# Performance work log

Hardware: AMD Instinct MI355X
Metric: run time of the kernel (lower is better)

The kernel has to match this reference:

```python
import jax, jax.numpy as jnp
import numpy as np

N, C, H, W = 8, 32, 256, 256
DEPTH = 4
PAD = (1, 1, 2, 2, 1, 1)  # (w_l, w_r, h_t, h_b, d_f, d_b)
K = 2  # pool kernel/stride along each of D,H,W
EPS = 1e-5


def setup_inputs() -> dict:
    key = jax.random.key(0)
    k1, k2, k3, k4, k5 = jax.random.split(key, 5)
    x = jax.random.normal(k1, (N, C, H, W), dtype=jnp.float32)
    gamma = jax.random.normal(k2, (C,), dtype=jnp.float32) * 0.1 + 1.0
    beta = jax.random.normal(k3, (C,), dtype=jnp.float32) * 0.1
    conv_w = jax.random.normal(k4, (C, C), dtype=jnp.float32) / np.sqrt(C)  # 1x1 conv [out,in]
    conv_b = jax.random.normal(k5, (C,), dtype=jnp.float32) * 0.1
    return {"x": x, "gamma": gamma, "beta": beta, "conv_w": conv_w, "conv_b": conv_b}


def _forward(x, gamma, beta, conv_w, conv_b):
    n, c, h, w = x.shape
    # InstanceNorm2d (affine, biased variance, eps=1e-5), stats per (N,C) over H,W
    mean = jnp.mean(x, axis=(2, 3), keepdims=True)
    var = jnp.mean(jnp.square(x - mean), axis=(2, 3), keepdims=True)
    xn = (x - mean) * jax.lax.rsqrt(var + EPS)
    xn = xn * gamma[None, :, None, None] + beta[None, :, None, None]
    # expand to 5D by repeating along depth
    x3 = jnp.broadcast_to(xn[:, :, None, :, :], (n, c, DEPTH, h, w))
    # ConstantPad3d with value 0.0
    wl, wr, ht, hb, df, db = PAD
    xp = jnp.pad(x3, ((0, 0), (0, 0), (df, db), (ht, hb), (wl, wr)))
    Dp, Hp, Wp = DEPTH + df + db, h + ht + hb, w + wl + wr  # all even by construction
    dq, hq, wq = Dp // K, Hp // K, Wp // K
    # block view: [n,c,dq,K,hq,K,wq,K] -> [n,c,dq,hq,wq,K*K*K] (row-major window order,
    # matching PyTorch's flattened pooling-window index order)
    blk = xp.reshape(n, c, dq, K, hq, K, wq, K).transpose(0, 1, 2, 4, 6, 3, 5, 7)
    blk = blk.reshape(n, c, dq, hq, wq, K * K * K)
    mx = jnp.max(blk, axis=-1)
    idx = jnp.argmax(blk, axis=-1)  # first occurrence on ties, like PyTorch CPU
    # MaxUnpool3d: scatter max back to its argmax position, zeros elsewhere
    unp_blk = jax.nn.one_hot(idx, K * K * K, dtype=x.dtype) * mx[..., None]
    unpooled = unp_blk.reshape(n, c, dq, hq, wq, K, K, K).transpose(0, 1, 2, 5, 3, 6, 4, 7)
    unpooled = unpooled.reshape(n, c, Dp, Hp, Wp)
    # crop padding, collapse depth via mean
    cropped = unpooled[:, :, df:df + DEPTH, ht:ht + h, wl:wl + w]
    collapsed = jnp.mean(cropped, axis=2)  # [n,c,h,w]
    # 1x1 conv + relu
    out = jnp.einsum('oc,nchw->nohw', conv_w, collapsed) + conv_b[None, :, None, None]
    return jax.nn.relu(out)


def reference(x, gamma, beta, conv_w, conv_b):
    return _forward(x, gamma, beta, conv_w, conv_b)
```

## Files before the change

kernel.cpp:

```cpp
#include <hip/hip_runtime.h>

#define N_   8
#define C_   32
#define H_   256
#define W_   256
#define HW_  (H_ * W_)

__global__ __launch_bounds__(1024) void stats_kernel(
    const float* __restrict__ x, const float* __restrict__ gamma,
    const float* __restrict__ beta, float2* __restrict__ ss)
{
    const int nc = blockIdx.x;
    const int t  = threadIdx.x;
    const float4* p = (const float4*)(x + (size_t)nc * HW_);

    float s0 = 0.f, s1 = 0.f, s2 = 0.f, s3 = 0.f;
    float q0 = 0.f, q1 = 0.f, q2 = 0.f, q3 = 0.f;
    #pragma unroll
    for (int i = 0; i < 16; ++i) {
        float4 v = p[t + (i << 10)];
        s0 += v.x; s1 += v.y; s2 += v.z; s3 += v.w;
        q0 = fmaf(v.x, v.x, q0); q1 = fmaf(v.y, v.y, q1);
        q2 = fmaf(v.z, v.z, q2); q3 = fmaf(v.w, v.w, q3);
    }
    double s = (double)s0 + (double)s1 + (double)s2 + (double)s3;
    double q = (double)q0 + (double)q1 + (double)q2 + (double)q3;
    #pragma unroll
    for (int off = 32; off > 0; off >>= 1) {
        s += __shfl_down(s, off);
        q += __shfl_down(q, off);
    }
    __shared__ double rs[16], rq[16];
    const int wid = t >> 6;
    if ((t & 63) == 0) { rs[wid] = s; rq[wid] = q; }
    __syncthreads();
    if (t == 0) {
        double S = 0.0, Q = 0.0;
        #pragma unroll
        for (int i = 0; i < 16; ++i) { S += rs[i]; Q += rq[i]; }
        double mean = S / (double)HW_;
        double var  = Q / (double)HW_ - mean * mean;
        double grs  = (double)gamma[nc & (C_ - 1)] / sqrt(var + 1e-5);
        float scale = (float)grs;
        float shift = (float)((double)beta[nc & (C_ - 1)] - mean * grs);
        ss[nc] = make_float2(scale, shift);
    }
}

__global__ __launch_bounds__(256, 8) void fused_kernel(
    const float* __restrict__ x, const float2* __restrict__ ss,
    const float* __restrict__ Wm, const float* __restrict__ bias,
    float* __restrict__ out)
{
    const int k   = blockIdx.x;
    const int qtr = blockIdx.y;
    const int n   = blockIdx.z;
    const int t   = threadIdx.x;
    const int w0  = qtr << 6;

    __shared__ float         sWT[C_][36];
    __shared__ float         sV[C_][34];
    __shared__ unsigned char sP[C_][36];

    #pragma unroll
    for (int r = 0; r < 4; ++r) {
        int i = t + (r << 8);
        sWT[i & 31][i >> 5] = Wm[i];
    }

    const int c  = t >> 3;
    const int li = t & 7;
    const float2 sc = ss[n * C_ + c];
    const float* plane = x + (size_t)(n * C_ + c) * HW_ + (size_t)(2 * k) * W_;
    const float* rowb  = plane + w0 + 8 * li;
    float4 u00 = ((const float4*)rowb)[0];
    float4 u01 = ((const float4*)rowb)[1];
    float4 u10 = ((const float4*)(rowb + W_))[0];
    float4 u11 = ((const float4*)(rowb + W_))[1];

    float bm = 0.f; int br = 0;
    {
        bool needL = (li == 0) && (qtr > 0);
        bool needR = (li == 7) && (qtr < 3);
        if (needL || needR) {
            const float* bp = plane + (needL ? (w0 - 1) : (w0 + 64));
            float p0 = fmaf(bp[0],  sc.x, sc.y);
            float p1 = fmaf(bp[W_], sc.x, sc.y);
            bm = fmaxf(p0, p1); br = (p1 > p0) ? 1 : 0;
        }
    }

    float vm[8];
    unsigned vr = 0;
    {
        float a0, a1;
        a0 = fmaf(u00.x, sc.x, sc.y); a1 = fmaf(u10.x, sc.x, sc.y);
        vm[0] = fmaxf(a0, a1); if (a1 > a0) vr |= 1u << 0;
        a0 = fmaf(u00.y, sc.x, sc.y); a1 = fmaf(u10.y, sc.x, sc.y);
        vm[1] = fmaxf(a0, a1); if (a1 > a0) vr |= 1u << 1;
        a0 = fmaf(u00.z, sc.x, sc.y); a1 = fmaf(u10.z, sc.x, sc.y);
        vm[2] = fmaxf(a0, a1); if (a1 > a0) vr |= 1u << 2;
        a0 = fmaf(u00.w, sc.x, sc.y); a1 = fmaf(u10.w, sc.x, sc.y);
        vm[3] = fmaxf(a0, a1); if (a1 > a0) vr |= 1u << 3;
        a0 = fmaf(u01.x, sc.x, sc.y); a1 = fmaf(u11.x, sc.x, sc.y);
        vm[4] = fmaxf(a0, a1); if (a1 > a0) vr |= 1u << 4;
        a0 = fmaf(u01.y, sc.x, sc.y); a1 = fmaf(u11.y, sc.x, sc.y);
        vm[5] = fmaxf(a0, a1); if (a1 > a0) vr |= 1u << 5;
        a0 = fmaf(u01.z, sc.x, sc.y); a1 = fmaf(u11.z, sc.x, sc.y);
        vm[6] = fmaxf(a0, a1); if (a1 > a0) vr |= 1u << 6;
        a0 = fmaf(u01.w, sc.x, sc.y); a1 = fmaf(u11.w, sc.x, sc.y);
        vm[7] = fmaxf(a0, a1); if (a1 > a0) vr |= 1u << 7;
    }

    const float pvm = __shfl_up(vm[7], 1);
    const int   pvr = __shfl_up((int)((vr >> 7) & 1u), 1);

    #pragma unroll
    for (int b = 0; b < 4; ++b) {
        float vL; int rL; bool padL = false;
        if (b == 0) {
            if (li == 0) {
                if (qtr == 0) { vL = 0.f; rL = 0; padL = true; }
                else          { vL = bm;  rL = br; }
            } else { vL = pvm; rL = pvr; }
        } else {
            vL = vm[2 * b - 1]; rL = (int)((vr >> (2 * b - 1)) & 1u);
        }
        float vR = vm[2 * b]; int rR = (int)((vr >> (2 * b)) & 1u);
        bool chooseL = (vL > vR) || ((vL == vR) && (rL <= rR));
        float m   = chooseL ? vL : vR;
        int   p   = chooseL ? (rL << 1) : ((rR << 1) | 1);
        float val = m * (m > 0.f ? 0.75f : 0.25f);
        if (chooseL && padL) val = 0.f;
        int jl = 4 * li + b;
        sV[c][jl] = val;
        sP[c][jl] = (unsigned char)p;
    }
    if (li == 7) {
        float vL = vm[7]; int rL = (int)((vr >> 7) & 1u);
        float vR; int rR; bool padR;
        if (qtr < 3) { vR = bm;  rR = br; padR = false; }
        else         { vR = 0.f; rR = 0;  padR = true;  }
        bool chooseL = (vL > vR) || ((vL == vR) && (rL <= rR));
        float m   = chooseL ? vL : vR;
        int   p   = chooseL ? (rL << 1) : ((rR << 1) | 1);
        float val = m * (m > 0.f ? 0.75f : 0.25f);
        if (!chooseL && padR) val = 0.f;
        sV[c][32] = val;
        sP[c][32] = (unsigned char)p;
    }
    __syncthreads();

    const int wv = t >> 6;
    const int ob = wv << 3;
    const int L  = t & 63;
    const int jl = (L + 1) >> 1;
    const int pm0 = (L & 1) ? 0 : 1;

    float acc0[8], acc1[8];
    #pragma unroll
    for (int oo = 0; oo < 8; ++oo) {
        float bo = bias[ob + oo];
        acc0[oo] = bo; acc1[oo] = bo;
    }

    #pragma unroll 8
    for (int cc = 0; cc < C_; ++cc) {
        float v = sV[cc][jl];
        int   p = sP[cc][jl];
        float m0 = (p == pm0)     ? v : 0.f;
        float m1 = (p == pm0 + 2) ? v : 0.f;
        float4 wa = *(const float4*)&sWT[cc][ob];
        float4 wb = *(const float4*)&sWT[cc][ob + 4];
        acc0[0] = fmaf(m0, wa.x, acc0[0]);
        acc0[1] = fmaf(m0, wa.y, acc0[1]);
        acc0[2] = fmaf(m0, wa.z, acc0[2]);
        acc0[3] = fmaf(m0, wa.w, acc0[3]);
        acc0[4] = fmaf(m0, wb.x, acc0[4]);
        acc0[5] = fmaf(m0, wb.y, acc0[5]);
        acc0[6] = fmaf(m0, wb.z, acc0[6]);
        acc0[7] = fmaf(m0, wb.w, acc0[7]);
        acc1[0] = fmaf(m1, wa.x, acc1[0]);
        acc1[1] = fmaf(m1, wa.y, acc1[1]);
        acc1[2] = fmaf(m1, wa.z, acc1[2]);
        acc1[3] = fmaf(m1, wa.w, acc1[3]);
        acc1[4] = fmaf(m1, wb.x, acc1[4]);
        acc1[5] = fmaf(m1, wb.y, acc1[5]);
        acc1[6] = fmaf(m1, wb.z, acc1[6]);
        acc1[7] = fmaf(m1, wb.w, acc1[7]);
    }

    float* obase = out + (size_t)(n * C_ + ob) * HW_
                       + (size_t)(2 * k) * W_ + w0 + L;
    #pragma unroll
    for (int oo = 0; oo < 8; ++oo) {
        obase[(size_t)oo * HW_]      = fmaxf(acc0[oo], 0.f);
        obase[(size_t)oo * HW_ + W_] = fmaxf(acc1[oo], 0.f);
    }
}

extern "C" void kernel_launch(void* const* d_in, const int* in_sizes, int n_in,
                              void* d_out, int out_size, void* d_ws, size_t ws_size,
                              hipStream_t stream) {
    const float* x     = (const float*)d_in[0];
    const float* gamma = (const float*)d_in[1];
    const float* beta  = (const float*)d_in[2];
    const float* Wm    = (const float*)d_in[3];
    const float* bias  = (const float*)d_in[4];
    float* out  = (float*)d_out;
    float2* ss  = (float2*)d_ws;

    stats_kernel<<<N_ * C_, 1024, 0, stream>>>(x, gamma, beta, ss);
    fused_kernel<<<dim3(H_ / 2, 4, N_), 256, 0, stream>>>(x, ss, Wm, bias, out);
}
```

Baseline: 138.0 us.

## Precompute raw-value pooling maxima in stats pass to halve second-pass input reads

The stats kernel now also does the vertical and horizontal 2-way max/argmax on the raw (un-normalized) input and writes a quarter-size intermediate, with the 2-bit window position packed into the low mantissa bits. The second kernel reads this compact buffer instead of the full input and applies the per-channel scale/shift afterward. This relies on the affine normalization preserving order, which requires a positive scale (gamma > 0). The intent is to cut pass-2 global reads of x by about 4x, at the cost of an extra workspace write and read and a small loss of mantissa precision.

```diff
diff --git a/kernel.cpp b/kernel.cpp
--- a/kernel.cpp
+++ b/kernel.cpp
@@ -5,26 +5,82 @@
 #define H_   256
 #define W_   256
 #define HW_  (H_ * W_)
+#define BROW_ 132
+#define B_OFF_ 1024
 
-__global__ __launch_bounds__(1024) void stats_kernel(
+__device__ __forceinline__ float pack_vp(float m, int pos) {
+    return __uint_as_float((__float_as_uint(m) & ~3u) | (unsigned)pos);
+}
+
+__global__ __launch_bounds__(1024) void pass1_kernel(
     const float* __restrict__ x, const float* __restrict__ gamma,
-    const float* __restrict__ beta, float2* __restrict__ ss)
+    const float* __restrict__ beta, float* __restrict__ ws)
 {
     const int nc = blockIdx.x;
     const int t  = threadIdx.x;
-    const float4* p = (const float4*)(x + (size_t)nc * HW_);
+    const int li = t & 31;
+    const int k0 = t >> 5;
+    const float* plane = x + (size_t)nc * HW_;
+    float* Bp = ws + B_OFF_ + (size_t)nc * (128 * BROW_);
 
-    float s0 = 0.f, s1 = 0.f, s2 = 0.f, s3 = 0.f;
-    float q0 = 0.f, q1 = 0.f, q2 = 0.f, q3 = 0.f;
+    float sx=0.f, sy=0.f, sz=0.f, sw=0.f;
+    float qx=0.f, qy=0.f, qz=0.f, qw=0.f;
+
     #pragma unroll
-    for (int i = 0; i < 16; ++i) {
-        float4 v = p[t + (i << 10)];
-        s0 += v.x; s1 += v.y; s2 += v.z; s3 += v.w;
-        q0 = fmaf(v.x, v.x, q0); q1 = fmaf(v.y, v.y, q1);
-        q2 = fmaf(v.z, v.z, q2); q3 = fmaf(v.w, v.w, q3);
+    for (int p = 0; p < 4; ++p) {
+        const int k = k0 + 32 * p;
+        const float* r0 = plane + (size_t)(2 * k) * W_ + 8 * li;
+        float4 a0 = ((const float4*)r0)[0];
+        float4 a1 = ((const float4*)r0)[1];
+        float4 b0 = ((const float4*)(r0 + W_))[0];
+        float4 b1 = ((const float4*)(r0 + W_))[1];
+
+        sx += a0.x + a1.x + b0.x + b1.x;
+        sy += a0.y + a1.y + b0.y + b1.y;
+        sz += a0.z + a1.z + b0.z + b1.z;
+        sw += a0.w + a1.w + b0.w + b1.w;
+        qx = fmaf(a0.x,a0.x,qx); qx = fmaf(a1.x,a1.x,qx);
+        qx = fmaf(b0.x,b0.x,qx); qx = fmaf(b1.x,b1.x,qx);
+        qy = fmaf(a0.y,a0.y,qy); qy = fmaf(a1.y,a1.y,qy);
+        qy = fmaf(b0.y,b0.y,qy); qy = fmaf(b1.y,b1.y,qy);
+        qz = fmaf(a0.z,a0.z,qz); qz = fmaf(a1.z,a1.z,qz);
+        qz = fmaf(b0.z,b0.z,qz); qz = fmaf(b1.z,b1.z,qz);
+        qw = fmaf(a0.w,a0.w,qw); qw = fmaf(a1.w,a1.w,qw);
+        qw = fmaf(b0.w,b0.w,qw); qw = fmaf(b1.w,b1.w,qw);
+
+        float vm0 = fmaxf(a0.x, b0.x); int r0b = (b0.x > a0.x) ? 1 : 0;
+        float vm1 = fmaxf(a0.y, b0.y); int r1b = (b0.y > a0.y) ? 1 : 0;
+        float vm2 = fmaxf(a0.z, b0.z); int r2b = (b0.z > a0.z) ? 1 : 0;
+        float vm3 = fmaxf(a0.w, b0.w); int r3b = (b0.w > a0.w) ? 1 : 0;
+        float vm4 = fmaxf(a1.x, b1.x); int r4b = (b1.x > a1.x) ? 1 : 0;
+        float vm5 = fmaxf(a1.y, b1.y); int r5b = (b1.y > a1.y) ? 1 : 0;
+        float vm6 = fmaxf(a1.z, b1.z); int r6b = (b1.z > a1.z) ? 1 : 0;
+        float vm7 = fmaxf(a1.w, b1.w); int r7b = (b1.w > a1.w) ? 1 : 0;
+
+        const float pvm = __shfl_up(vm7, 1);
+        const int   pvr = __shfl_up(r7b, 1);
+
+        float f0, f1, f2, f3;
+        if (li == 0) {
+            f0 = pack_vp(vm0, (r0b << 1) | 1);
+        } else {
+            bool cl = (pvm > vm0) || ((pvm == vm0) && (pvr <= r0b));
+            f0 = cl ? pack_vp(pvm, pvr << 1) : pack_vp(vm0, (r0b << 1) | 1);
+        }
+        { bool cl = (vm1 > vm2) || ((vm1 == vm2) && (r1b <= r2b));
+          f1 = cl ? pack_vp(vm1, r1b << 1) : pack_vp(vm2, (r2b << 1) | 1); }
+        { bool cl = (vm3 > vm4) || ((vm3 == vm4) && (r3b <= r4b));
+          f2 = cl ? pack_vp(vm3, r3b << 1) : pack_vp(vm4, (r4b << 1) | 1); }
+        { bool cl = (vm5 > vm6) || ((vm5 == vm6) && (r5b <= r6b));
+          f3 = cl ? pack_vp(vm5, r5b << 1) : pack_vp(vm6, (r6b << 1) | 1); }
+
+        *(float4*)(Bp + (size_t)k * BROW_ + 4 * li) = make_float4(f0, f1, f2, f3);
+        if (li == 31)
+            Bp[(size_t)k * BROW_ + 128] = pack_vp(vm7, r7b << 1);
     }
-    double s = (double)s0 + (double)s1 + (double)s2 + (double)s3;
-    double q = (double)q0 + (double)q1 + (double)q2 + (double)q3;
+
+    double s = (double)sx + (double)sy + (double)sz + (double)sw;
+    double q = (double)qx + (double)qy + (double)qz + (double)qw;
     #pragma unroll
     for (int off = 32; off > 0; off >>= 1) {
         s += __shfl_down(s, off);
@@ -41,121 +97,46 @@
         double mean = S / (double)HW_;
         double var  = Q / (double)HW_ - mean * mean;
         double grs  = (double)gamma[nc & (C_ - 1)] / sqrt(var + 1e-5);
-        float scale = (float)grs;
-        float shift = (float)((double)beta[nc & (C_ - 1)] - mean * grs);
-        ss[nc] = make_float2(scale, shift);
+        ((float2*)ws)[nc] = make_float2((float)grs,
+                                        (float)((double)beta[nc & (C_ - 1)] - mean * grs));
     }
 }
 
-__global__ __launch_bounds__(256, 8) void fused_kernel(
-    const float* __restrict__ x, const float2* __restrict__ ss,
-    const float* __restrict__ Wm, const float* __restrict__ bias,
-    float* __restrict__ out)
+__global__ __launch_bounds__(256, 8) void pass2_kernel(
+    const float* __restrict__ ws, const float* __restrict__ Wm,
+    const float* __restrict__ bias, float* __restrict__ out)
 {
     const int k   = blockIdx.x;
     const int qtr = blockIdx.y;
     const int n   = blockIdx.z;
     const int t   = threadIdx.x;
-    const int w0  = qtr << 6;
 
-    __shared__ float         sWT[C_][36];
-    __shared__ float         sV[C_][34];
-    __shared__ unsigned char sP[C_][36];
+    __shared__ float  sWT[C_][36];
+    __shared__ float  sB[C_][36];
+    __shared__ float2 sSS[C_];
 
     #pragma unroll
     for (int r = 0; r < 4; ++r) {
         int i = t + (r << 8);
         sWT[i & 31][i >> 5] = Wm[i];
     }
+    if (t < C_) sSS[t] = ((const float2*)ws)[n * C_ + t];
 
-    const int c  = t >> 3;
-    const int li = t & 7;
-    const float2 sc = ss[n * C_ + c];
-    const float* plane = x + (size_t)(n * C_ + c) * HW_ + (size_t)(2 * k) * W_;
-    const float* rowb  = plane + w0 + 8 * li;
-    float4 u00 = ((const float4*)rowb)[0];
-    float4 u01 = ((const float4*)rowb)[1];
-    float4 u10 = ((const float4*)(rowb + W_))[0];
-    float4 u11 = ((const float4*)(rowb + W_))[1];
-
-    float bm = 0.f; int br = 0;
-    {
-        bool needL = (li == 0) && (qtr > 0);
-        bool needR = (li == 7) && (qtr < 3);
-        if (needL || needR) {
-            const float* bp = plane + (needL ? (w0 - 1) : (w0 + 64));
-            float p0 = fmaf(bp[0],  sc.x, sc.y);
-            float p1 = fmaf(bp[W_], sc.x, sc.y);
-            bm = fmaxf(p0, p1); br = (p1 > p0) ? 1 : 0;
-        }
-    }
-
-    float vm[8];
-    unsigned vr = 0;
-    {
-        float a0, a1;
-        a0 = fmaf(u00.x, sc.x, sc.y); a1 = fmaf(u10.x, sc.x, sc.y);
-        vm[0] = fmaxf(a0, a1); if (a1 > a0) vr |= 1u << 0;
-        a0 = fmaf(u00.y, sc.x, sc.y); a1 = fmaf(u10.y, sc.x, sc.y);
-        vm[1] = fmaxf(a0, a1); if (a1 > a0) vr |= 1u << 1;
-        a0 = fmaf(u00.z, sc.x, sc.y); a1 = fmaf(u10.z, sc.x, sc.y);
-        vm[2] = fmaxf(a0, a1); if (a1 > a0) vr |= 1u << 2;
-        a0 = fmaf(u00.w, sc.x, sc.y); a1 = fmaf(u10.w, sc.x, sc.y);
-        vm[3] = fmaxf(a0, a1); if (a1 > a0) vr |= 1u << 3;
-        a0 = fmaf(u01.x, sc.x, sc.y); a1 = fmaf(u11.x, sc.x, sc.y);
-        vm[4] = fmaxf(a0, a1); if (a1 > a0) vr |= 1u << 4;
-        a0 = fmaf(u01.y, sc.x, sc.y); a1 = fmaf(u11.y, sc.x, sc.y);
-        vm[5] = fmaxf(a0, a1); if (a1 > a0) vr |= 1u << 5;
-        a0 = fmaf(u01.z, sc.x, sc.y); a1 = fmaf(u11.z, sc.x, sc.y);
-        vm[6] = fmaxf(a0, a1); if (a1 > a0) vr |= 1u << 6;
-        a0 = fmaf(u01.w, sc.x, sc.y); a1 = fmaf(u11.w, sc.x, sc.y);
-        vm[7] = fmaxf(a0, a1); if (a1 > a0) vr |= 1u << 7;
-    }
-
-    const float pvm = __shfl_up(vm[7], 1);
-    const int   pvr = __shfl_up((int)((vr >> 7) & 1u), 1);
-
-    #pragma unroll
-    for (int b = 0; b < 4; ++b) {
-        float vL; int rL; bool padL = false;
-        if (b == 0) {
-            if (li == 0) {
-                if (qtr == 0) { vL = 0.f; rL = 0; padL = true; }
-                else          { vL = bm;  rL = br; }
-            } else { vL = pvm; rL = pvr; }
-        } else {
-            vL = vm[2 * b - 1]; rL = (int)((vr >> (2 * b - 1)) & 1u);
-        }
-        float vR = vm[2 * b]; int rR = (int)((vr >> (2 * b)) & 1u);
-        bool chooseL = (vL > vR) || ((vL == vR) && (rL <= rR));
-        float m   = chooseL ? vL : vR;
-        int   p   = chooseL ? (rL << 1) : ((rR << 1) | 1);
-        float val = m * (m > 0.f ? 0.75f : 0.25f);
-        if (chooseL && padL) val = 0.f;
-        int jl = 4 * li + b;
-        sV[c][jl] = val;
-        sP[c][jl] = (unsigned char)p;
-    }
-    if (li == 7) {
-        float vL = vm[7]; int rL = (int)((vr >> 7) & 1u);
-        float vR; int rR; bool padR;
-        if (qtr < 3) { vR = bm;  rR = br; padR = false; }
-        else         { vR = 0.f; rR = 0;  padR = true;  }
-        bool chooseL = (vL > vR) || ((vL == vR) && (rL <= rR));
-        float m   = chooseL ? vL : vR;
-        int   p   = chooseL ? (rL << 1) : ((rR << 1) | 1);
-        float val = m * (m > 0.f ? 0.75f : 0.25f);
-        if (!chooseL && padR) val = 0.f;
-        sV[c][32] = val;
-        sP[c][32] = (unsigned char)p;
+    const float4* B4 = (const float4*)(ws + B_OFF_);
+    for (int i = t; i < 288; i += 256) {
+        int c = i / 9, f = i - 9 * c;
+        ((float4*)&sB[c][0])[f] =
+            B4[(size_t)((n * C_ + c) * 128 + k) * 33 + qtr * 8 + f];
     }
     __syncthreads();
 
-    const int wv = t >> 6;
-    const int ob = wv << 3;
-    const int L  = t & 63;
-    const int jl = (L + 1) >> 1;
-    const int pm0 = (L & 1) ? 0 : 1;
+    const int wv  = t >> 6;
+    const int ob  = wv << 3;
+    const int Ll  = t & 63;
+    const int jl  = (Ll + 1) >> 1;
+    const int pm0 = (Ll & 1) ? 0 : 1;
+    const bool bnd = (qtr == 0 && Ll == 0) || (qtr == 3 && Ll == 63);
+    const float negc = bnd ? 0.f : 0.25f;
 
     float acc0[8], acc1[8];
     #pragma unroll
@@ -166,10 +147,13 @@
 
     #pragma unroll 8
     for (int cc = 0; cc < C_; ++cc) {
-        float v = sV[cc][jl];
-        int   p = sP[cc][jl];
-        float m0 = (p == pm0)     ? v : 0.f;
-        float m1 = (p == pm0 + 2) ? v : 0.f;
+        float2 sc = sSS[cc];
+        float pv  = sB[cc][jl];
+        int  pos  = (int)(__float_as_uint(pv) & 3u);
+        float vn  = fmaf(pv, sc.x, sc.y);
+        float val = vn * ((vn > 0.f) ? 0.75f : negc);
+        float m0  = (pos == pm0)     ? val : 0.f;
+        float m1  = (pos == pm0 + 2) ? val : 0.f;
         float4 wa = *(const float4*)&sWT[cc][ob];
         float4 wb = *(const float4*)&sWT[cc][ob + 4];
         acc0[0] = fmaf(m0, wa.x, acc0[0]);
@@ -191,7 +175,7 @@
     }
 
     float* obase = out + (size_t)(n * C_ + ob) * HW_
-                       + (size_t)(2 * k) * W_ + w0 + L;
+                       + (size_t)(2 * k) * W_ + (qtr << 6) + Ll;
     #pragma unroll
     for (int oo = 0; oo < 8; ++oo) {
         obase[(size_t)oo * HW_]      = fmaxf(acc0[oo], 0.f);
@@ -207,9 +191,9 @@
     const float* beta  = (const float*)d_in[2];
     const float* Wm    = (const float*)d_in[3];
     const float* bias  = (const float*)d_in[4];
-    float* out  = (float*)d_out;
-    float2* ss  = (float2*)d_ws;
+    float* out = (float*)d_out;
+    float* ws  = (float*)d_ws;
 
-    stats_kernel<<<N_ * C_, 1024, 0, stream>>>(x, gamma, beta, ss);
-    fused_kernel<<<dim3(H_ / 2, 4, N_), 256, 0, stream>>>(x, ss, Wm, bias, out);
+    pass1_kernel<<<N_ * C_, 1024, 0, stream>>>(x, gamma, beta, ws);
+    pass2_kernel<<<dim3(H_ / 2, 4, N_), 256, 0, stream>>>(ws, Wm, bias, out);
 }
```

Result: no change. 138.8 us (+0.6%).
